# Kernel tuning notes

Measured on AMD Instinct MI355X. Metric: run time of the kernel, lower is better.

The kernel has to match this reference:

```python
import jax, jax.numpy as jnp
import numpy as np

B, T = 4, 2048
IN_H, OUT_H = 4096, 4096   # in_hidden_size = output features, out_hidden_size = input features (torch F.linear quirk)
RANK = 1024


def setup_inputs() -> dict:
    key = jax.random.key(0)
    kx, ku, ks, kv, kb = jax.random.split(key, 5)
    x = jax.random.normal(kx, (B, T, OUT_H), dtype=jnp.float32)
    U = jax.random.normal(ku, (IN_H, RANK), dtype=jnp.float32) * 0.02
    S = jax.random.uniform(ks, (RANK,), dtype=jnp.float32)
    V = jax.random.normal(kv, (OUT_H, RANK), dtype=jnp.float32) * 0.02
    bias = jax.random.normal(kb, (IN_H,), dtype=jnp.float32) * 0.01
    return {"x": x, "U": U, "S": S, "V": V, "bias": bias}


def reference(x, U, S, V, bias):
    # Faithful to torch: M = U @ diag(S) @ V.T  (shape [in_hidden, out_hidden]);
    # F.linear(x, M, bias) = x @ M.T + bias, so x:[...,out_hidden] -> out:[...,in_hidden]
    M = (U * S) @ V.T                     # [IN_H, OUT_H]; (U*S) == U @ diag(S)
    return jnp.einsum('bto,io->bti', x, M) + bias
```

## Files before the change

kernel.cpp:

```cpp
#include <hip/hip_runtime.h>
#include <stdint.h>

typedef __attribute__((ext_vector_type(4))) float  floatx4;
typedef __attribute__((ext_vector_type(8))) short  short8;
typedef __attribute__((ext_vector_type(8))) __bf16 bf16x8;

__device__ __forceinline__ unsigned short f2bf(float f) {
  unsigned int u = __builtin_bit_cast(unsigned int, f);
  u += 0x7fffu + ((u >> 16) & 1u);
  return (unsigned short)(u >> 16);
}

__global__ __launch_bounds__(256) void cast_x_kernel(const float* __restrict__ X,
                                                     unsigned short* __restrict__ Xb) {
  size_t i = ((size_t)blockIdx.x * 256 + threadIdx.x) * 8;
  const floatx4* p = (const floatx4*)(X + i);
  floatx4 a = p[0], b = p[1];
  union { unsigned short us[8]; short8 v; } o;
  o.us[0] = f2bf(a[0]); o.us[1] = f2bf(a[1]); o.us[2] = f2bf(a[2]); o.us[3] = f2bf(a[3]);
  o.us[4] = f2bf(b[0]); o.us[5] = f2bf(b[1]); o.us[6] = f2bf(b[2]); o.us[7] = f2bf(b[3]);
  *(short8*)(Xb + i) = o.v;
}

__global__ __launch_bounds__(256) void transpose_v_kernel(const float* __restrict__ V,
                                                          unsigned short* __restrict__ Vt,
                                                          int rows, int cols) {
  __shared__ float tile[32][33];
  int bx = blockIdx.x * 32;
  int by = blockIdx.y * 32;
  int tx = threadIdx.x & 31;
  int ty = threadIdx.x >> 5;
  for (int i = ty; i < 32; i += 8)
    tile[i][tx] = V[(size_t)(by + i) * cols + bx + tx];
  __syncthreads();
  for (int i = ty; i < 32; i += 8)
    Vt[(size_t)(bx + i) * rows + by + tx] = f2bf(tile[tx][i]);
}

__global__ __launch_bounds__(256) void prep_u_kernel(const float* __restrict__ U,
                                                     const float* __restrict__ S,
                                                     unsigned short* __restrict__ Ub,
                                                     unsigned int rankMask) {
  size_t i = ((size_t)blockIdx.x * 256 + threadIdx.x) * 4;
  floatx4 u = *(const floatx4*)(U + i);
  floatx4 s = *(const floatx4*)(S + (i & (size_t)rankMask));
  union { unsigned short us[4]; unsigned long long v; } o;
  o.us[0] = f2bf(u[0] * s[0]); o.us[1] = f2bf(u[1] * s[1]);
  o.us[2] = f2bf(u[2] * s[2]); o.us[3] = f2bf(u[3] * s[3]);
  *(unsigned long long*)(Ub + i) = o.v;
}

template <bool STORE_BF16>
__global__ __launch_bounds__(256, 2)
void gemm_bt_kernel(const unsigned short* __restrict__ A,
                    const unsigned short* __restrict__ Bt,
                    void* __restrict__ Cv,
                    const float* __restrict__ bias,
                    int M, int N, int K) {
  __shared__ unsigned short sA[128 * 32];
  __shared__ unsigned short sB[128 * 32];

  const int tid  = threadIdx.x;
  const int lane = tid & 63;
  const int wave = tid >> 6;
  const int wm = (wave >> 1) * 64;
  const int wn = (wave & 1) * 64;
  const int row0 = blockIdx.y * 128;
  const int col0 = blockIdx.x * 128;

  floatx4 acc[4][4];
  for (int i = 0; i < 4; ++i)
    for (int j = 0; j < 4; ++j)
      acc[i][j] = (floatx4){0.f, 0.f, 0.f, 0.f};

  const unsigned short* Ablk = A + (size_t)row0 * K;
  const unsigned short* Bblk = Bt + (size_t)col0 * K;

  const int r0 = tid >> 2,         c0 = (tid & 3) * 8;
  const int r1 = (256 + tid) >> 2, c1 = (tid & 3) * 8;
  const int base0 = (wave * 64) * 8;
  const int base1 = (256 + wave * 64) * 8;

  const int mrow = lane & 15;
  const int quad = lane >> 4;

  typedef const __attribute__((address_space(1))) void* gptr_t;
  typedef __attribute__((address_space(3))) void*       lptr_t;

  for (int k0 = 0; k0 < K; k0 += 32) {
    __builtin_amdgcn_global_load_lds((gptr_t)(Ablk + (size_t)r0 * K + k0 + c0),
                                     (lptr_t)(sA + base0), 16, 0, 0);
    __builtin_amdgcn_global_load_lds((gptr_t)(Ablk + (size_t)r1 * K + k0 + c1),
                                     (lptr_t)(sA + base1), 16, 0, 0);
    __builtin_amdgcn_global_load_lds((gptr_t)(Bblk + (size_t)r0 * K + k0 + c0),
                                     (lptr_t)(sB + base0), 16, 0, 0);
    __builtin_amdgcn_global_load_lds((gptr_t)(Bblk + (size_t)r1 * K + k0 + c1),
                                     (lptr_t)(sB + base1), 16, 0, 0);
    __syncthreads();

    bf16x8 af[4], bfr[4];
#pragma unroll
    for (int mi = 0; mi < 4; ++mi)
      af[mi] = __builtin_bit_cast(bf16x8,
                *(const short8*)(sA + (wm + mi * 16 + mrow) * 32 + quad * 8));
#pragma unroll
    for (int ni = 0; ni < 4; ++ni)
      bfr[ni] = __builtin_bit_cast(bf16x8,
                *(const short8*)(sB + (wn + ni * 16 + mrow) * 32 + quad * 8));
#pragma unroll
    for (int mi = 0; mi < 4; ++mi)
#pragma unroll
      for (int ni = 0; ni < 4; ++ni)
        acc[mi][ni] = __builtin_amdgcn_mfma_f32_16x16x32_bf16(af[mi], bfr[ni],
                                                              acc[mi][ni], 0, 0, 0);
    __syncthreads();
  }

  const int orow = row0 + wm + quad * 4;
  const int ocol = col0 + wn + mrow;
  if (STORE_BF16) {
    unsigned short* C = (unsigned short*)Cv;
#pragma unroll
    for (int mi = 0; mi < 4; ++mi)
#pragma unroll
      for (int r = 0; r < 4; ++r) {
        size_t rowoff = (size_t)(orow + mi * 16 + r) * N;
#pragma unroll
        for (int ni = 0; ni < 4; ++ni)
          C[rowoff + ocol + ni * 16] = f2bf(acc[mi][ni][r]);
      }
  } else {
    float* C = (float*)Cv;
    float bv[4];
#pragma unroll
    for (int ni = 0; ni < 4; ++ni) bv[ni] = bias[ocol + ni * 16];
#pragma unroll
    for (int mi = 0; mi < 4; ++mi)
#pragma unroll
      for (int r = 0; r < 4; ++r) {
        size_t rowoff = (size_t)(orow + mi * 16 + r) * N;
#pragma unroll
        for (int ni = 0; ni < 4; ++ni)
          C[rowoff + ocol + ni * 16] = acc[mi][ni][r] + bv[ni];
      }
  }
}

extern "C" void kernel_launch(void* const* d_in, const int* in_sizes, int n_in,
                              void* d_out, int out_size, void* d_ws, size_t ws_size,
                              hipStream_t stream) {
  const float* x    = (const float*)d_in[0];
  const float* U    = (const float*)d_in[1];
  const float* S    = (const float*)d_in[2];
  const float* V    = (const float*)d_in[3];
  const float* bias = (const float*)d_in[4];

  const int RANK = in_sizes[2];
  const int INH  = in_sizes[4];
  const int OUTH = in_sizes[3] / RANK;
  const int M    = in_sizes[0] / OUTH;

  unsigned short* Xb = (unsigned short*)d_ws;
  unsigned short* Vt = Xb + (size_t)M * OUTH;
  unsigned short* Ub = Vt + (size_t)RANK * OUTH;
  unsigned short* Yb = Ub + (size_t)INH * RANK;

  cast_x_kernel<<<(int)(((size_t)M * OUTH) / 2048), 256, 0, stream>>>(x, Xb);
  transpose_v_kernel<<<dim3(RANK / 32, OUTH / 32), 256, 0, stream>>>(V, Vt, OUTH, RANK);
  prep_u_kernel<<<(int)(((size_t)INH * RANK) / 1024), 256, 0, stream>>>(U, S, Ub,
                                                                        (unsigned)(RANK - 1));
  gemm_bt_kernel<true><<<dim3(RANK / 128, M / 128), 256, 0, stream>>>(
      Xb, Vt, (void*)Yb, nullptr, M, RANK, OUTH);
  gemm_bt_kernel<false><<<dim3(INH / 128, M / 128), 256, 0, stream>>>(
      Yb, Ub, d_out, bias, M, INH, RANK);
}
```

Baseline: 430.4 us.

## Use narrower N tile for first GEMM and grouped block swizzle for L2 reuse

The GEMM kernel gains a template parameter for the N tile width. The first GEMM (K=4096, N=1024) now uses 128x64 tiles, which doubles its block count from 512 to 1024 to fill the CUs better. Both GEMMs switch to a 1D grid remapped so that groups of 8 row-tiles walk across column tiles together, which should improve L2 reuse of the A and B panels. The narrower tile lowers arithmetic intensity per block and adds more redundant A loads.

```diff
diff --git a/kernel.cpp b/kernel.cpp
--- a/kernel.cpp
+++ b/kernel.cpp
@@ -50,27 +50,34 @@
   *(unsigned long long*)(Ub + i) = o.v;
 }
 
-template <bool STORE_BF16>
+template <int WN_TILES, int GXSHIFT, bool STORE_BF16>
 __global__ __launch_bounds__(256, 2)
 void gemm_bt_kernel(const unsigned short* __restrict__ A,
                     const unsigned short* __restrict__ Bt,
                     void* __restrict__ Cv,
                     const float* __restrict__ bias,
-                    int M, int N, int K) {
+                    int N, int K) {
+  constexpr int BN = WN_TILES * 32;
   __shared__ unsigned short sA[128 * 32];
-  __shared__ unsigned short sB[128 * 32];
+  __shared__ unsigned short sB[BN * 32];
+
+  unsigned bid  = blockIdx.x;
+  unsigned band = bid >> (3 + GXSHIFT);
+  unsigned rem  = bid & ((8u << GXSHIFT) - 1u);
+  unsigned by   = (band << 3) | (rem & 7u);
+  unsigned bx   = rem >> 3;
 
   const int tid  = threadIdx.x;
   const int lane = tid & 63;
   const int wave = tid >> 6;
   const int wm = (wave >> 1) * 64;
-  const int wn = (wave & 1) * 64;
-  const int row0 = blockIdx.y * 128;
-  const int col0 = blockIdx.x * 128;
+  const int wn = (wave & 1) * (WN_TILES * 16);
+  const int row0 = by * 128;
+  const int col0 = bx * BN;
 
-  floatx4 acc[4][4];
+  floatx4 acc[4][WN_TILES];
   for (int i = 0; i < 4; ++i)
-    for (int j = 0; j < 4; ++j)
+    for (int j = 0; j < WN_TILES; ++j)
       acc[i][j] = (floatx4){0.f, 0.f, 0.f, 0.f};
 
   const unsigned short* Ablk = A + (size_t)row0 * K;
@@ -94,23 +101,24 @@
                                      (lptr_t)(sA + base1), 16, 0, 0);
     __builtin_amdgcn_global_load_lds((gptr_t)(Bblk + (size_t)r0 * K + k0 + c0),
                                      (lptr_t)(sB + base0), 16, 0, 0);
-    __builtin_amdgcn_global_load_lds((gptr_t)(Bblk + (size_t)r1 * K + k0 + c1),
-                                     (lptr_t)(sB + base1), 16, 0, 0);
+    if constexpr (BN == 128)
+      __builtin_amdgcn_global_load_lds((gptr_t)(Bblk + (size_t)r1 * K + k0 + c1),
+                                       (lptr_t)(sB + base1), 16, 0, 0);
     __syncthreads();
 
-    bf16x8 af[4], bfr[4];
+    bf16x8 af[4], bfr[WN_TILES];
 #pragma unroll
     for (int mi = 0; mi < 4; ++mi)
       af[mi] = __builtin_bit_cast(bf16x8,
                 *(const short8*)(sA + (wm + mi * 16 + mrow) * 32 + quad * 8));
 #pragma unroll
-    for (int ni = 0; ni < 4; ++ni)
+    for (int ni = 0; ni < WN_TILES; ++ni)
       bfr[ni] = __builtin_bit_cast(bf16x8,
                 *(const short8*)(sB + (wn + ni * 16 + mrow) * 32 + quad * 8));
 #pragma unroll
     for (int mi = 0; mi < 4; ++mi)
 #pragma unroll
-      for (int ni = 0; ni < 4; ++ni)
+      for (int ni = 0; ni < WN_TILES; ++ni)
         acc[mi][ni] = __builtin_amdgcn_mfma_f32_16x16x32_bf16(af[mi], bfr[ni],
                                                               acc[mi][ni], 0, 0, 0);
     __syncthreads();
@@ -126,21 +134,21 @@
       for (int r = 0; r < 4; ++r) {
         size_t rowoff = (size_t)(orow + mi * 16 + r) * N;
 #pragma unroll
-        for (int ni = 0; ni < 4; ++ni)
+        for (int ni = 0; ni < WN_TILES; ++ni)
           C[rowoff + ocol + ni * 16] = f2bf(acc[mi][ni][r]);
       }
   } else {
     float* C = (float*)Cv;
-    float bv[4];
+    float bv[WN_TILES];
 #pragma unroll
-    for (int ni = 0; ni < 4; ++ni) bv[ni] = bias[ocol + ni * 16];
+    for (int ni = 0; ni < WN_TILES; ++ni) bv[ni] = bias[ocol + ni * 16];
 #pragma unroll
     for (int mi = 0; mi < 4; ++mi)
 #pragma unroll
       for (int r = 0; r < 4; ++r) {
         size_t rowoff = (size_t)(orow + mi * 16 + r) * N;
 #pragma unroll
-        for (int ni = 0; ni < 4; ++ni)
+        for (int ni = 0; ni < WN_TILES; ++ni)
           C[rowoff + ocol + ni * 16] = acc[mi][ni][r] + bv[ni];
       }
   }
@@ -169,8 +177,10 @@
   transpose_v_kernel<<<dim3(RANK / 32, OUTH / 32), 256, 0, stream>>>(V, Vt, OUTH, RANK);
   prep_u_kernel<<<(int)(((size_t)INH * RANK) / 1024), 256, 0, stream>>>(U, S, Ub,
                                                                         (unsigned)(RANK - 1));
-  gemm_bt_kernel<true><<<dim3(RANK / 128, M / 128), 256, 0, stream>>>(
-      Xb, Vt, (void*)Yb, nullptr, M, RANK, OUTH);
-  gemm_bt_kernel<false><<<dim3(INH / 128, M / 128), 256, 0, stream>>>(
-      Yb, Ub, d_out, bias, M, INH, RANK);
+
+  gemm_bt_kernel<2, 4, true><<<(RANK / 64) * (M / 128), 256, 0, stream>>>(
+      Xb, Vt, (void*)Yb, nullptr, RANK, OUTH);
+
+  gemm_bt_kernel<4, 5, false><<<(INH / 128) * (M / 128), 256, 0, stream>>>(
+      Yb, Ub, d_out, bias, INH, RANK);
 }
```

Result: no change. 427.1 us (-0.8%).
